# Performance work log

Measured on AMD Instinct MI355X. Metric: run time of the kernel, lower is better.

## Reference

```python
import jax, jax.numpy as jnp
import numpy as np

TAU = 2.0         # LIFNode default tau
VTH = 1.0         # v_threshold
ALPHA = 2.0       # ATan surrogate alpha
TIME_STEP = 4     # hard-coded in RecurrentLIFNode
NUM_LAYERS = 4
HIDDEN = 512
INPUT = 512
T, B = 128, 512

@jax.custom_vjp
def atan_spike(x):
    # heaviside forward, ATan surrogate backward (spikingjelly surrogate.ATan)
    return (x >= 0.0).astype(x.dtype)

def _atan_fwd(x):
    return atan_spike(x), x

def _atan_bwd(x, g):
    return (g * (ALPHA / 2.0) / (1.0 + (jnp.pi / 2.0 * ALPHA * x) ** 2),)

atan_spike.defvjp(_atan_fwd, _atan_bwd)

def lif_burst(v, inp):
    # run one LIFCell time_step times with fixed input `inp`, accumulate averages
    acc_v = jnp.zeros_like(v)
    acc_s = jnp.zeros_like(v)
    for _ in range(TIME_STEP):
        v = v + (inp - v) / TAU          # neuronal_charge (decay_input=True, v_reset=None)
        s = atan_spike(v - VTH)          # neuronal_fire
        v = v - s * VTH                  # soft reset (v_reset=None)
        acc_v = acc_v + v
        acc_s = acc_s + s
    return v, acc_v / TIME_STEP, acc_s / TIME_STEP


def setup_inputs() -> dict:
    key = jax.random.key(0)
    k1, k2, k3 = jax.random.split(key, 3)
    x = jax.random.normal(k1, (T, B, INPUT), dtype=jnp.float32)
    bound = 1.0 / np.sqrt(INPUT)
    W = jax.random.uniform(k2, (HIDDEN, INPUT), dtype=jnp.float32, minval=-bound, maxval=bound)
    b = jax.random.uniform(k3, (HIDDEN,), dtype=jnp.float32, minval=-bound, maxval=bound)
    return {"x": x, "W": W, "b": b}


def reference(x, W, b):
    # x: [T, B, input]; project once (linear_ih)
    xp = jnp.einsum('tbi,hi->tbh', x, W) + b   # [T, B, H]
    Bsz, H = x.shape[1], W.shape[0]
    init_state = jnp.zeros((NUM_LAYERS, Bsz, H), dtype=x.dtype)  # current_state persists across t

    def step(cur, xt):
        curs = [cur[i] for i in range(NUM_LAYERS)]
        y = xt
        new_vs = []
        last_spk = None
        for i in range(NUM_LAYERS):
            curs[i], avg_v, avg_s = lif_burst(curs[i], y)
            new_vs.append(avg_v)
            y = avg_v          # next layer consumes averaged membrane state
            last_spk = avg_s
        return jnp.stack(curs), (last_spk, jnp.stack(new_vs))

    _, (out, states_seq) = jax.lax.scan(step, init_state, xp)
    # out: [T, B, H] averaged spikes of last layer; final new_states_list: [L, B, H]
    return out, states_seq[-1]
```

## Files before the change

kernel.cpp:

```cpp
#include <hip/hip_runtime.h>
#include <stdint.h>

#define TT 128
#define BSZ 512
#define HID 512
#define KDIM 512
#define BH (BSZ*HID)

__global__ __launch_bounds__(256, 1) void gemm_f32(
    const float* __restrict__ A, const float* __restrict__ W,
    const float* __restrict__ bias, float* __restrict__ C) {
  __shared__ float As[2][16][132];
  __shared__ float Bs[2][16][260];
  const int t  = threadIdx.x;
  const int m0 = blockIdx.y * 128;
  const int n0 = blockIdx.x * 256;
  const int tx = t & 15;
  const int ty = t >> 4;
  const int r0 = t >> 2;
  const int kg = t & 3;

  float acc[8][16];
  #pragma unroll
  for (int i = 0; i < 8; ++i)
    #pragma unroll
    for (int j = 0; j < 16; ++j) acc[i][j] = 0.f;

  const float* Ap = A + (size_t)(m0 + r0) * KDIM + kg * 4;
  const float* Wp = W + (size_t)(n0 + r0) * KDIM + kg * 4;

  float4 a0 = *(const float4*)Ap;
  float4 a1 = *(const float4*)(Ap + (size_t)64  * KDIM);
  float4 w0 = *(const float4*)Wp;
  float4 w1 = *(const float4*)(Wp + (size_t)64  * KDIM);
  float4 w2 = *(const float4*)(Wp + (size_t)128 * KDIM);
  float4 w3 = *(const float4*)(Wp + (size_t)192 * KDIM);

  #define STAGE(BUF) do { \
    As[BUF][kg*4+0][r0]     = a0.x; As[BUF][kg*4+1][r0]     = a0.y; \
    As[BUF][kg*4+2][r0]     = a0.z; As[BUF][kg*4+3][r0]     = a0.w; \
    As[BUF][kg*4+0][r0+64]  = a1.x; As[BUF][kg*4+1][r0+64]  = a1.y; \
    As[BUF][kg*4+2][r0+64]  = a1.z; As[BUF][kg*4+3][r0+64]  = a1.w; \
    Bs[BUF][kg*4+0][r0]     = w0.x; Bs[BUF][kg*4+1][r0]     = w0.y; \
    Bs[BUF][kg*4+2][r0]     = w0.z; Bs[BUF][kg*4+3][r0]     = w0.w; \
    Bs[BUF][kg*4+0][r0+64]  = w1.x; Bs[BUF][kg*4+1][r0+64]  = w1.y; \
    Bs[BUF][kg*4+2][r0+64]  = w1.z; Bs[BUF][kg*4+3][r0+64]  = w1.w; \
    Bs[BUF][kg*4+0][r0+128] = w2.x; Bs[BUF][kg*4+1][r0+128] = w2.y; \
    Bs[BUF][kg*4+2][r0+128] = w2.z; Bs[BUF][kg*4+3][r0+128] = w2.w; \
    Bs[BUF][kg*4+0][r0+192] = w3.x; Bs[BUF][kg*4+1][r0+192] = w3.y; \
    Bs[BUF][kg*4+2][r0+192] = w3.z; Bs[BUF][kg*4+3][r0+192] = w3.w; \
  } while (0)

  STAGE(0);

  int cur = 0;
  for (int k0 = 0; k0 < KDIM; k0 += 16) {
    __syncthreads();
    const bool more = (k0 + 16 < KDIM);
    if (more) {
      a0 = *(const float4*)(Ap + k0 + 16);
      a1 = *(const float4*)(Ap + (size_t)64  * KDIM + k0 + 16);
      w0 = *(const float4*)(Wp + k0 + 16);
      w1 = *(const float4*)(Wp + (size_t)64  * KDIM + k0 + 16);
      w2 = *(const float4*)(Wp + (size_t)128 * KDIM + k0 + 16);
      w3 = *(const float4*)(Wp + (size_t)192 * KDIM + k0 + 16);
    }

    #pragma unroll
    for (int kk = 0; kk < 16; ++kk) {
      const float4 xa0 = *(const float4*)&As[cur][kk][ty*8];
      const float4 xa1 = *(const float4*)&As[cur][kk][ty*8 + 4];
      const float a[8] = {xa0.x,xa0.y,xa0.z,xa0.w,xa1.x,xa1.y,xa1.z,xa1.w};
      #pragma unroll
      for (int q = 0; q < 4; ++q) {
        const float4 xb = *(const float4*)&Bs[cur][kk][64*q + tx*4];
        #pragma unroll
        for (int i = 0; i < 8; ++i) {
          acc[i][q*4+0] = __builtin_fmaf(a[i], xb.x, acc[i][q*4+0]);
          acc[i][q*4+1] = __builtin_fmaf(a[i], xb.y, acc[i][q*4+1]);
          acc[i][q*4+2] = __builtin_fmaf(a[i], xb.z, acc[i][q*4+2]);
          acc[i][q*4+3] = __builtin_fmaf(a[i], xb.w, acc[i][q*4+3]);
        }
      }
    }

    if (more) {
      const int nb = cur ^ 1;
      STAGE(nb);
    }
    cur ^= 1;
  }
  #undef STAGE

  float4 bv[4];
  #pragma unroll
  for (int q = 0; q < 4; ++q) bv[q] = *(const float4*)&bias[n0 + 64*q + tx*4];
  #pragma unroll
  for (int i = 0; i < 8; ++i) {
    float* cp = C + (size_t)(m0 + ty*8 + i) * HID + n0 + tx*4;
    #pragma unroll
    for (int q = 0; q < 4; ++q) {
      const float4 v = {acc[i][q*4+0] + bv[q].x, acc[i][q*4+1] + bv[q].y,
                        acc[i][q*4+2] + bv[q].z, acc[i][q*4+3] + bv[q].w};
      *(float4*)(cp + 64*q) = v;
    }
  }
}

__device__ __forceinline__ float lif_step(float y, float v[4], float av[4]) {
  float as3 = 0.f;
  #pragma unroll
  for (int l = 0; l < 4; ++l) {
    float vv = v[l];
    float accv = 0.f, accs = 0.f;
    #pragma unroll
    for (int k = 0; k < 4; ++k) {
      const float d = y - vv;
      vv = __builtin_fmaf(d, 0.5f, vv);
      const float spk = (vv >= 1.0f) ? 1.0f : 0.0f;
      vv -= spk;
      accv += vv;
      accs += spk;
    }
    v[l] = vv;
    const float a = accv * 0.25f;
    av[l] = a;
    y = a;
    as3 = accs;
  }
  return as3;
}

__global__ __launch_bounds__(256) void lif_scan(
    const float* __restrict__ xp, float* __restrict__ outp, float* __restrict__ vstate,
    int tc, int first, int last) {
  const int idx = blockIdx.x * 256 + threadIdx.x;
  float v[4];
  if (first) {
    #pragma unroll
    for (int l = 0; l < 4; ++l) v[l] = 0.f;
  } else {
    #pragma unroll
    for (int l = 0; l < 4; ++l) v[l] = vstate[(size_t)l * BH + idx];
  }
  float av[4] = {0.f, 0.f, 0.f, 0.f};
  const float* p = xp + idx;
  float* op = outp + idx;

  if ((tc & 3) == 0 && tc >= 8) {
    float curb[4];
    #pragma unroll
    for (int i = 0; i < 4; ++i) curb[i] = p[(size_t)i * BH];
    for (int t = 0; t + 4 < tc; t += 4) {
      float nxtb[4];
      #pragma unroll
      for (int i = 0; i < 4; ++i) nxtb[i] = p[(size_t)(i + 4) * BH];
      #pragma unroll
      for (int i = 0; i < 4; ++i) {
        const float as3 = lif_step(curb[i], v, av);
        op[(size_t)i * BH] = as3 * 0.25f;
      }
      #pragma unroll
      for (int i = 0; i < 4; ++i) curb[i] = nxtb[i];
      p += 4 * BH; op += 4 * BH;
    }
    #pragma unroll
    for (int i = 0; i < 4; ++i) {
      const float as3 = lif_step(curb[i], v, av);
      op[(size_t)i * BH] = as3 * 0.25f;
    }
  } else {
    for (int t = 0; t < tc; ++t) {
      const float as3 = lif_step(p[0], v, av);
      *op = as3 * 0.25f;
      p += BH; op += BH;
    }
  }

  if (last) {
    #pragma unroll
    for (int l = 0; l < 4; ++l) vstate[(size_t)l * BH + idx] = av[l];
  } else {
    #pragma unroll
    for (int l = 0; l < 4; ++l) vstate[(size_t)l * BH + idx] = v[l];
  }
}

extern "C" void kernel_launch(void* const* d_in, const int* in_sizes, int n_in,
                              void* d_out, int out_size, void* d_ws, size_t ws_size,
                              hipStream_t stream) {
  const float* x = (const float*)d_in[0];
  const float* W = (const float*)d_in[1];
  const float* b = (const float*)d_in[2];
  float* out    = (float*)d_out;
  float* states = out + (size_t)TT * BH;

  int tc = TT;
  while (tc > 1 && (size_t)tc * BH * 4ull > ws_size) tc >>= 1;
  float* xp = (float*)d_ws;
  const int nc = TT / tc;

  for (int c = 0; c < nc; ++c) {
    hipLaunchKernelGGL(gemm_f32, dim3(HID / 256, tc * BSZ / 128), dim3(256), 0, stream,
                       x + (size_t)c * tc * BH, W, b, xp);
    hipLaunchKernelGGL(lif_scan, dim3(BH / 256), dim3(256), 0, stream,
                       xp, out + (size_t)c * tc * BH, states,
                       tc, c == 0 ? 1 : 0, c == nc - 1 ? 1 : 0);
  }
}
```

Baseline: 608.5 us.

## Pipeline LIF layers across lanes with shuffle handoff

Restructures the LIF scan so each neuron uses four lanes, one per layer, with the layers pipelined over time steps and activations passed between lanes via __shfl_up. This shortens the per-step serial dependency chain and quadruples thread-level parallelism. Output spikes use nontemporal stores. The cost is a pipeline fill/drain of three extra steps, narrower coalesced loads (16 distinct addresses per wave) and shuffle overhead.

```diff
diff --git a/kernel.cpp b/kernel.cpp
--- a/kernel.cpp
+++ b/kernel.cpp
@@ -107,83 +107,58 @@
   }
 }
 
-__device__ __forceinline__ float lif_step(float y, float v[4], float av[4]) {
-  float as3 = 0.f;
-  #pragma unroll
-  for (int l = 0; l < 4; ++l) {
-    float vv = v[l];
-    float accv = 0.f, accs = 0.f;
-    #pragma unroll
-    for (int k = 0; k < 4; ++k) {
-      const float d = y - vv;
-      vv = __builtin_fmaf(d, 0.5f, vv);
-      const float spk = (vv >= 1.0f) ? 1.0f : 0.0f;
-      vv -= spk;
-      accv += vv;
-      accs += spk;
-    }
-    v[l] = vv;
-    const float a = accv * 0.25f;
-    av[l] = a;
-    y = a;
-    as3 = accs;
-  }
-  return as3;
-}
-
 __global__ __launch_bounds__(256) void lif_scan(
     const float* __restrict__ xp, float* __restrict__ outp, float* __restrict__ vstate,
     int tc, int first, int last) {
-  const int idx = blockIdx.x * 256 + threadIdx.x;
-  float v[4];
-  if (first) {
-    #pragma unroll
-    for (int l = 0; l < 4; ++l) v[l] = 0.f;
-  } else {
-    #pragma unroll
-    for (int l = 0; l < 4; ++l) v[l] = vstate[(size_t)l * BH + idx];
+  const int t    = threadIdx.x;
+  const int lane = t & 63;
+  const int l    = lane & 3;
+  const int nidx = blockIdx.x * 64 + (t >> 6) * 16 + (lane >> 2);
+  const float* px = xp + nidx;
+  float* op = outp + nidx;
+
+  float v    = 0.f;
+  if (!first) v = vstate[(size_t)l * BH + nidx];
+  float avr  = 0.f;
+  float hand = 0.f;
+
+  float xq[4];
+  #pragma unroll
+  for (int i = 0; i < 4; ++i) xq[i] = px[(size_t)(i < tc ? i : 0) * BH];
+
+  const int S = tc + 3;
+
+  #define LSTEP(J) do { \
+    const int s = s0 + (J); \
+    const float y0 = xq[J]; \
+    { const int sp = s + 4; if (sp < tc) xq[J] = px[(size_t)sp * BH]; } \
+    const float y = (l == 0) ? y0 : hand; \
+    float vv = v, accv = 0.f, accs = 0.f; \
+    _Pragma("unroll") \
+    for (int k = 0; k < 4; ++k) { \
+      const float d = y - vv;                         \
+      vv = __builtin_fmaf(d, 0.5f, vv);               \
+      const float spk = (vv >= 1.0f) ? 1.0f : 0.0f;   \
+      vv -= spk;                                      \
+      accv += vv; \
+      accs += spk; \
+    } \
+    const float av_new = accv * 0.25f;                \
+    const bool act = (s >= l) && ((s - l) < tc); \
+    v   = act ? vv : v; \
+    avr = act ? av_new : avr; \
+    hand = __shfl_up(avr, 1, 4); \
+    if (l == 3 && act) \
+      __builtin_nontemporal_store(accs * 0.25f, op + (size_t)(s - 3) * BH); \
+  } while (0)
+
+  for (int s0 = 0; s0 < S; s0 += 4) {
+    LSTEP(0); LSTEP(1); LSTEP(2); LSTEP(3);
   }
-  float av[4] = {0.f, 0.f, 0.f, 0.f};
-  const float* p = xp + idx;
-  float* op = outp + idx;
+  #undef LSTEP
 
-  if ((tc & 3) == 0 && tc >= 8) {
-    float curb[4];
-    #pragma unroll
-    for (int i = 0; i < 4; ++i) curb[i] = p[(size_t)i * BH];
-    for (int t = 0; t + 4 < tc; t += 4) {
-      float nxtb[4];
-      #pragma unroll
-      for (int i = 0; i < 4; ++i) nxtb[i] = p[(size_t)(i + 4) * BH];
-      #pragma unroll
-      for (int i = 0; i < 4; ++i) {
-        const float as3 = lif_step(curb[i], v, av);
-        op[(size_t)i * BH] = as3 * 0.25f;
-      }
-      #pragma unroll
-      for (int i = 0; i < 4; ++i) curb[i] = nxtb[i];
-      p += 4 * BH; op += 4 * BH;
-    }
-    #pragma unroll
-    for (int i = 0; i < 4; ++i) {
-      const float as3 = lif_step(curb[i], v, av);
-      op[(size_t)i * BH] = as3 * 0.25f;
-    }
-  } else {
-    for (int t = 0; t < tc; ++t) {
-      const float as3 = lif_step(p[0], v, av);
-      *op = as3 * 0.25f;
-      p += BH; op += BH;
-    }
-  }
-
-  if (last) {
-    #pragma unroll
-    for (int l = 0; l < 4; ++l) vstate[(size_t)l * BH + idx] = av[l];
-  } else {
-    #pragma unroll
-    for (int l = 0; l < 4; ++l) vstate[(size_t)l * BH + idx] = v[l];
-  }
+  if (last) vstate[(size_t)l * BH + nidx] = avr;
+  else      vstate[(size_t)l * BH + nidx] = v;
 }
 
 extern "C" void kernel_launch(void* const* d_in, const int* in_sizes, int n_in,
@@ -203,7 +178,7 @@
   for (int c = 0; c < nc; ++c) {
     hipLaunchKernelGGL(gemm_f32, dim3(HID / 256, tc * BSZ / 128), dim3(256), 0, stream,
                        x + (size_t)c * tc * BH, W, b, xp);
-    hipLaunchKernelGGL(lif_scan, dim3(BH / 256), dim3(256), 0, stream,
+    hipLaunchKernelGGL(lif_scan, dim3(BH / 64), dim3(256), 0, stream,
                        xp, out + (size_t)c * tc * BH, states,
                        tc, c == 0 ? 1 : 0, c == nc - 1 ? 1 : 0);
   }
```

Result: slower. 685.5 us (+12.7%).
